# Optimization experiments

Hardware: AMD Instinct MI355X
Metric: run time of the kernel (lower is better)

Reference implementation:

```python
import jax, jax.numpy as jnp
import numpy as np
import math


def setup_inputs() -> dict:
    key = jax.random.key(0)
    ks = jax.random.split(key, 5)
    B, L, H = 16384, 336, 168
    T = L + H
    T_air = jax.random.normal(ks[0], (B, T), dtype=jnp.float32) * 8.0 + 10.0
    T_obs = T_air + jax.random.normal(ks[1], (B, T), dtype=jnp.float32) * 2.0
    wind = jax.random.uniform(ks[2], (B, T), dtype=jnp.float32) * 10.0
    par = jax.random.uniform(ks[3], (B, T), dtype=jnp.float32) * 500.0
    dt = jax.random.uniform(ks[4], (B, T), dtype=jnp.float32) * 3600.0 + 1800.0
    k_init = 1e-4
    k_raw = jnp.float32(k_init + math.log(-math.expm1(-k_init)))  # softplus inverse
    return {
        "T_obs": T_obs, "T_air": T_air, "wind": wind, "par": par, "dt": dt,
        "L_hist": L,
        "k_raw": k_raw,
        "log_q": jnp.float32(-8.0), "log_r": jnp.float32(-4.0),
        "log_p0": jnp.float32(-2.0), "log_q_scale": jnp.float32(0.0),
        "theta_par_lin": jnp.float32(1e-5), "theta_par_quad": jnp.float32(1e-8),
        "theta_wind_cool": jnp.float32(-1e-5), "theta_sensible": jnp.float32(-1e-6),
        "theta_forced_conv": jnp.float32(-1e-7),
    }


def reference(T_obs, T_air, wind, par, dt, L_hist, k_raw, log_q, log_r, log_p0,
              log_q_scale, theta_par_lin, theta_par_quad, theta_wind_cool,
              theta_sensible, theta_forced_conv):
    B, T_total = T_obs.shape
    L = int(L_hist)
    H = T_total - L

    k = jax.nn.softplus(k_raw)
    q = jnp.exp(log_q)
    q_scale = jnp.exp(log_q_scale)
    R = jnp.exp(log_r)
    P0 = jnp.exp(log_p0)

    def predict(T, P, Ta, w, p, dtt):
        dT = T - Ta
        cl = (theta_par_lin * p + theta_par_quad * p * p + theta_wind_cool * w
              + theta_sensible * dT + theta_forced_conv * w * dT)
        T_pred = jnp.clip(T - k * dT * dtt + cl * dtt, -50.0, 100.0)
        F = jnp.clip(1.0 - k * dtt + (theta_sensible + theta_forced_conv * w) * dtt, -2.0, 2.0)
        P_pred = jnp.clip(F * F * P + q_scale * q * dtt, 1e-10, 1e6)
        return T_pred, P_pred

    def filt_step(carry, xs):
        T, P = carry
        Ta, w, p, dtt, y = xs
        Tp, Pp = predict(T, P, Ta, w, p, dtt)
        S = Pp + R
        K = Pp / S
        T_upd = Tp + K * (y - Tp)
        P_upd = (1.0 - K) ** 2 * Pp + K * K * R
        return (T_upd, P_upd), None

    s0 = T_obs[:, 0]
    P0b = jnp.broadcast_to(P0, (B,)).astype(T_obs.dtype)

    # filtering over t = 1 .. L-1 (forcing from t-1, dt/obs at t)
    filt_xs = (T_air[:, :L - 1].T, wind[:, :L - 1].T, par[:, :L - 1].T,
               jnp.clip(dt[:, 1:L], 1.0, None).T, T_obs[:, 1:L].T)
    (s, P), _ = jax.lax.scan(filt_step, (s0, P0b), filt_xs)

    def fcst_step(carry, xs):
        T, P = carry
        Ta, w, p, dtt = xs
        Tp, Pp = predict(T, P, Ta, w, p, dtt)
        return (Tp, Pp), (Tp, Pp)

    # open-loop forecast over t = L .. L+H-1 (forcing from idx-1)
    fcst_xs = (T_air[:, L - 1:L + H - 1].T, wind[:, L - 1:L + H - 1].T,
               par[:, L - 1:L + H - 1].T, jnp.clip(dt[:, L:], 1.0, None).T)
    _, (T_preds, T_vars) = jax.lax.scan(fcst_step, (s, P), fcst_xs)

    return T_preds.T, T_vars.T  # each [B, H]
```

## Files before the change

### kernel.cpp

```cpp
#include <hip/hip_runtime.h>
#include <hip/hip_fp16.h>

namespace {
constexpr int kB = 16384;
constexpr int kL = 336;
constexpr int kH = 168;
constexpr int kT = 504;
constexpr int kW = 16;
constexpr int kNW = 32;
constexpr int kFW = 21;
constexpr int kIS = 66;
constexpr int kITile = kW * kIS;
constexpr int kOS = 17;
constexpr int kOTile = 64 * kOS;
}

__device__ inline void fwait(int* f, int target) {
    int guard = 0;
    while (__hip_atomic_load(f, __ATOMIC_ACQUIRE, __HIP_MEMORY_SCOPE_WORKGROUP) < target) {
        __builtin_amdgcn_s_sleep(1);
        if (++guard > (1 << 22)) break;
    }
}
__device__ inline void fpost(int* f, int lane) {
    __threadfence_block();
    if (lane == 0) atomicAdd(f, 1);
}

__global__ __launch_bounds__(256, 1)
void kf_fused(const float* __restrict__ g_obs,
              const float* __restrict__ g_air,
              const float* __restrict__ g_wind,
              const float* __restrict__ g_par,
              const float* __restrict__ g_dt,
              const float* __restrict__ s_k_raw,
              const float* __restrict__ s_log_q,
              const float* __restrict__ s_log_r,
              const float* __restrict__ s_log_p0,
              const float* __restrict__ s_log_qs,
              const float* __restrict__ s_th_pl,
              const float* __restrict__ s_th_pq,
              const float* __restrict__ s_th_wc,
              const float* __restrict__ s_th_s,
              const float* __restrict__ s_th_fc,
              float* __restrict__ out)
{
    __shared__ __half s_in[5][2][kITile];
    __shared__ float  s_oT[2][kOTile];
    __shared__ float  s_oV[2][kOTile];
    __shared__ int    s_flag[8];

    const int tid = threadIdx.x, wid = tid >> 6, lane = tid & 63;
    const int b0 = blockIdx.x * 64;

    if (tid < 8) s_flag[tid] = 0;
    __syncthreads();

    int* pcAW = &s_flag[0];
    int* pcPD = &s_flag[1];
    int* pcY  = &s_flag[2];
    int* cc   = &s_flag[3];
    int* sc   = &s_flag[4];

    if (wid == 1 || wid == 2) {
        const float* g0 = (wid == 1) ? g_air  : g_par;
        const float* g1 = (wid == 1) ? g_wind : g_dt;
        __half* base0 = (wid == 1) ? &s_in[0][0][0] : &s_in[2][0][0];
        __half* base1 = (wid == 1) ? &s_in[1][0][0] : &s_in[3][0][0];
        int* pc = (wid == 1) ? pcAW : pcPD;
        const int rloc = lane >> 4, trel = lane & 15;
        for (int w = 0; w < kNW; ++w) {
            if (w >= 2) fwait(cc, w - 1);
            const int bi = w & 1;
            int t = w * kW + trel; if (t > kT - 1) t = kT - 1;
            float v0[16], v1[16];
#pragma unroll
            for (int i = 0; i < 16; ++i) {
                const size_t off = (size_t)(b0 + 4 * i + rloc) * kT + t;
                v0[i] = g0[off];
                v1[i] = g1[off];
            }
            __half* d0 = base0 + bi * kITile;
            __half* d1 = base1 + bi * kITile;
#pragma unroll
            for (int i = 0; i < 16; ++i) {
                const int idx = trel * kIS + 4 * i + rloc;
                d0[idx] = __float2half(v0[i]);
                d1[idx] = __float2half(v1[i]);
            }
            fpost(pc, lane);
        }
    } else if (wid == 3) {
        const int rloc = lane >> 4, trel = lane & 15;
        for (int w = 0; w < kFW; ++w) {
            if (w >= 2) fwait(cc, w - 1);
            const int bi = w & 1;
            const int t = w * kW + trel;
            float v[16];
#pragma unroll
            for (int i = 0; i < 16; ++i)
                v[i] = g_obs[(size_t)(b0 + 4 * i + rloc) * kT + t];
            __half* d = &s_in[4][bi][0];
#pragma unroll
            for (int i = 0; i < 16; ++i)
                d[trel * kIS + 4 * i + rloc] = __float2half(v[i]);
            fpost(pcY, lane);
        }
        const int rq = lane & 3, rr = lane >> 2;
        float* outT = out;
        float* outV = out + (size_t)kB * kH;
        for (int w = kFW; w < kNW; ++w) {
            fwait(cc, w + 1);
            const int bi = w & 1;
            const int h0 = (w - kFW) * kW;
            const int nq = (w == kNW - 1) ? 2 : 4;
#pragma unroll
            for (int i = 0; i < 4; ++i) {
                const int r = 16 * i + rr;
                if (rq < nq) {
                    const float4 tv = *(const float4*)&s_oT[bi][r * kOS + rq * 4];
                    const float4 vv = *(const float4*)&s_oV[bi][r * kOS + rq * 4];
                    *(float4*)&outT[(size_t)(b0 + r) * kH + h0 + rq * 4] = tv;
                    *(float4*)&outV[(size_t)(b0 + r) * kH + h0 + rq * 4] = vv;
                }
            }
            fpost(sc, lane);
        }
    } else {
        const float kpar = log1pf(expf(s_k_raw[0]));
        const float qq   = expf(s_log_q[0]) * expf(s_log_qs[0]);
        const float R    = expf(s_log_r[0]);
        float P          = expf(s_log_p0[0]);
        const float th_pl = s_th_pl[0], th_pq = s_th_pq[0], th_wc = s_th_wc[0];
        const float th_s  = s_th_s[0],  th_fc = s_th_fc[0];
        float Tst = 0.0f, aC = 0.0f, wC = 0.0f, pC = 0.0f;

        for (int w = 0; w < kNW; ++w) {
            const int bi = w & 1;
            fwait(pcAW, w + 1);
            fwait(pcPD, w + 1);
            if (w < kFW) fwait(pcY, w + 1);
            if (w >= kFW + 2) fwait(sc, w - (kFW + 1));

            const __half* A  = &s_in[0][bi][0];
            const __half* Wd = &s_in[1][bi][0];
            const __half* Pr = &s_in[2][bi][0];
            const __half* Dd = &s_in[3][bi][0];
            const __half* Yy = &s_in[4][bi][0];

            if (w < kFW) {
                int trel = 0;
                if (w == 0) {
                    Tst = __half2float(Yy[lane]);
                    aC  = __half2float(A[lane]);
                    wC  = __half2float(Wd[lane]);
                    pC  = __half2float(Pr[lane]);
                    trel = 1;
                }
                for (; trel < kW; ++trel) {
                    const int ix = trel * kIS + lane;
                    const float dtt = fmaxf(__half2float(Dd[ix]), 1.0f);
                    const float y   = __half2float(Yy[ix]);
                    const float a   = __half2float(A[ix]);
                    const float wv  = __half2float(Wd[ix]);
                    const float pv  = __half2float(Pr[ix]);
                    const float dT  = Tst - aC;
                    const float gk  = fmaf(th_fc, wC, th_s) - kpar;
                    const float base = fmaf(pC, fmaf(th_pq, pC, th_pl), th_wc * wC);
                    const float Tp = fminf(fmaxf(fmaf(fmaf(gk, dT, base), dtt, Tst), -50.0f), 100.0f);
                    const float F  = fminf(fmaxf(fmaf(gk, dtt, 1.0f), -2.0f), 2.0f);
                    const float Pp = fminf(fmaxf(fmaf(F * F, P, qq * dtt), 1e-10f), 1e6f);
                    const float Kg = Pp * __builtin_amdgcn_rcpf(Pp + R);
                    Tst = fmaf(Kg, y - Tp, Tp);
                    const float omk = 1.0f - Kg;
                    P = fmaf(omk * omk, Pp, Kg * Kg * R);
                    aC = a; wC = wv; pC = pv;
                }
            } else {
                float* oT = &s_oT[bi][lane * kOS];
                float* oV = &s_oV[bi][lane * kOS];
#pragma unroll
                for (int trel = 0; trel < kW; ++trel) {
                    const int ix = trel * kIS + lane;
                    const float dtt = fmaxf(__half2float(Dd[ix]), 1.0f);
                    const float a   = __half2float(A[ix]);
                    const float wv  = __half2float(Wd[ix]);
                    const float pv  = __half2float(Pr[ix]);
                    const float dT  = Tst - aC;
                    const float gk  = fmaf(th_fc, wC, th_s) - kpar;
                    const float base = fmaf(pC, fmaf(th_pq, pC, th_pl), th_wc * wC);
                    Tst = fminf(fmaxf(fmaf(fmaf(gk, dT, base), dtt, Tst), -50.0f), 100.0f);
                    const float F = fminf(fmaxf(fmaf(gk, dtt, 1.0f), -2.0f), 2.0f);
                    P = fminf(fmaxf(fmaf(F * F, P, qq * dtt), 1e-10f), 1e6f);
                    oT[trel] = Tst;
                    oV[trel] = P;
                    aC = a; wC = wv; pC = pv;
                }
            }
            fpost(cc, lane);
        }
    }
}

extern "C" void kernel_launch(void* const* d_in, const int* in_sizes, int n_in,
                              void* d_out, int out_size, void* d_ws, size_t ws_size,
                              hipStream_t stream) {
    const float* g_obs  = (const float*)d_in[0];
    const float* g_air  = (const float*)d_in[1];
    const float* g_wind = (const float*)d_in[2];
    const float* g_par  = (const float*)d_in[3];
    const float* g_dt   = (const float*)d_in[4];
    const float* k_raw  = (const float*)d_in[6];
    const float* log_q  = (const float*)d_in[7];
    const float* log_r  = (const float*)d_in[8];
    const float* log_p0 = (const float*)d_in[9];
    const float* log_qs = (const float*)d_in[10];
    const float* th_pl  = (const float*)d_in[11];
    const float* th_pq  = (const float*)d_in[12];
    const float* th_wc  = (const float*)d_in[13];
    const float* th_s   = (const float*)d_in[14];
    const float* th_fc  = (const float*)d_in[15];
    float* out = (float*)d_out;

    dim3 grid(kB / 64), block(256);
    hipLaunchKernelGGL(kf_fused, grid, block, 0, stream,
                       g_obs, g_air, g_wind, g_par, g_dt,
                       k_raw, log_q, log_r, log_p0, log_qs,
                       th_pl, th_pq, th_wc, th_s, th_fc, out);
}
```

Measured before the change: 220.5 us.

## Prefetch inputs two windows ahead with float4 loads and relax flag fences

Loader wavefronts now issue float4 global loads for the next two time windows into registers before waiting, so global latency overlaps with the compute wave's work. Shared staging moves from fp16 to fp32, which removes the conversions and the precision loss but doubles LDS use. The workgroup fences and acquire loads on the flags are replaced with relaxed atomics plus an explicit lgkmcnt wait and compiler barriers, which cuts synchronisation overhead but relies on those ordering assumptions being correct.

```diff
diff --git a/kernel.cpp b/kernel.cpp
--- a/kernel.cpp
+++ b/kernel.cpp
@@ -1,5 +1,4 @@
 #include <hip/hip_runtime.h>
-#include <hip/hip_fp16.h>
 
 namespace {
 constexpr int kB = 16384;
@@ -17,14 +16,16 @@
 
 __device__ inline void fwait(int* f, int target) {
     int guard = 0;
-    while (__hip_atomic_load(f, __ATOMIC_ACQUIRE, __HIP_MEMORY_SCOPE_WORKGROUP) < target) {
+    while (__hip_atomic_load(f, __ATOMIC_RELAXED, __HIP_MEMORY_SCOPE_WORKGROUP) < target) {
         __builtin_amdgcn_s_sleep(1);
         if (++guard > (1 << 22)) break;
     }
+    asm volatile("" ::: "memory");
 }
 __device__ inline void fpost(int* f, int lane) {
-    __threadfence_block();
-    if (lane == 0) atomicAdd(f, 1);
+    asm volatile("s_waitcnt lgkmcnt(0)" ::: "memory");
+    if (lane == 0)
+        __hip_atomic_fetch_add(f, 1, __ATOMIC_RELAXED, __HIP_MEMORY_SCOPE_WORKGROUP);
 }
 
 __global__ __launch_bounds__(256, 1)
@@ -45,10 +46,10 @@
               const float* __restrict__ s_th_fc,
               float* __restrict__ out)
 {
-    __shared__ __half s_in[5][2][kITile];
-    __shared__ float  s_oT[2][kOTile];
-    __shared__ float  s_oV[2][kOTile];
-    __shared__ int    s_flag[8];
+    __shared__ float s_in[5][2][kITile];
+    __shared__ float s_oT[2][kOTile];
+    __shared__ float s_oV[2][kOTile];
+    __shared__ int   s_flag[8];
 
     const int tid = threadIdx.x, wid = tid >> 6, lane = tid & 63;
     const int b0 = blockIdx.x * 64;
@@ -62,49 +63,68 @@
     int* cc   = &s_flag[3];
     int* sc   = &s_flag[4];
 
+    const int iq = lane & 3;
+    const int ir = lane >> 2;
+
+    auto issue = [&](const float* __restrict__ g, int w, float4* r) {
+        int t = w * kW + iq * 4;
+        if (t > kT - 4) t = kT - 4;
+#pragma unroll
+        for (int i = 0; i < 4; ++i)
+            r[i] = *(const float4*)(g + (size_t)(b0 + 16 * i + ir) * kT + t);
+    };
+    auto stash = [&](const float4* r, float* dst) {
+        const int tb = iq * 4;
+#pragma unroll
+        for (int i = 0; i < 4; ++i) {
+            const int row = 16 * i + ir;
+            dst[(tb + 0) * kIS + row] = r[i].x;
+            dst[(tb + 1) * kIS + row] = r[i].y;
+            dst[(tb + 2) * kIS + row] = r[i].z;
+            dst[(tb + 3) * kIS + row] = r[i].w;
+        }
+    };
+
     if (wid == 1 || wid == 2) {
         const float* g0 = (wid == 1) ? g_air  : g_par;
         const float* g1 = (wid == 1) ? g_wind : g_dt;
-        __half* base0 = (wid == 1) ? &s_in[0][0][0] : &s_in[2][0][0];
-        __half* base1 = (wid == 1) ? &s_in[1][0][0] : &s_in[3][0][0];
+        float* base0 = (wid == 1) ? &s_in[0][0][0] : &s_in[2][0][0];
+        float* base1 = (wid == 1) ? &s_in[1][0][0] : &s_in[3][0][0];
         int* pc = (wid == 1) ? pcAW : pcPD;
-        const int rloc = lane >> 4, trel = lane & 15;
+
+        float4 a0[4], b0r[4], a1[4], b1r[4];
+        issue(g0, 0, a0); issue(g1, 0, b0r);
+        issue(g0, 1, a1); issue(g1, 1, b1r);
+        __builtin_amdgcn_sched_barrier(0);
         for (int w = 0; w < kNW; ++w) {
             if (w >= 2) fwait(cc, w - 1);
-            const int bi = w & 1;
-            int t = w * kW + trel; if (t > kT - 1) t = kT - 1;
-            float v0[16], v1[16];
-#pragma unroll
-            for (int i = 0; i < 16; ++i) {
-                const size_t off = (size_t)(b0 + 4 * i + rloc) * kT + t;
-                v0[i] = g0[off];
-                v1[i] = g1[off];
-            }
-            __half* d0 = base0 + bi * kITile;
-            __half* d1 = base1 + bi * kITile;
-#pragma unroll
-            for (int i = 0; i < 16; ++i) {
-                const int idx = trel * kIS + 4 * i + rloc;
-                d0[idx] = __float2half(v0[i]);
-                d1[idx] = __float2half(v1[i]);
-            }
-            fpost(pc, lane);
+            if (w & 1) {
+                stash(a1, base0 + kITile); stash(b1r, base1 + kITile);
+                fpost(pc, lane);
+                if (w + 2 < kNW) { issue(g0, w + 2, a1); issue(g1, w + 2, b1r); }
+            } else {
+                stash(a0, base0); stash(b0r, base1);
+                fpost(pc, lane);
+                if (w + 2 < kNW) { issue(g0, w + 2, a0); issue(g1, w + 2, b0r); }
+            }
+            __builtin_amdgcn_sched_barrier(0);
         }
     } else if (wid == 3) {
-        const int rloc = lane >> 4, trel = lane & 15;
+        float4 y0[4], y1[4];
+        issue(g_obs, 0, y0); issue(g_obs, 1, y1);
+        __builtin_amdgcn_sched_barrier(0);
         for (int w = 0; w < kFW; ++w) {
             if (w >= 2) fwait(cc, w - 1);
-            const int bi = w & 1;
-            const int t = w * kW + trel;
-            float v[16];
-#pragma unroll
-            for (int i = 0; i < 16; ++i)
-                v[i] = g_obs[(size_t)(b0 + 4 * i + rloc) * kT + t];
-            __half* d = &s_in[4][bi][0];
-#pragma unroll
-            for (int i = 0; i < 16; ++i)
-                d[trel * kIS + 4 * i + rloc] = __float2half(v[i]);
-            fpost(pcY, lane);
+            if (w & 1) {
+                stash(y1, &s_in[4][1][0]);
+                fpost(pcY, lane);
+                if (w + 2 < kFW) issue(g_obs, w + 2, y1);
+            } else {
+                stash(y0, &s_in[4][0][0]);
+                fpost(pcY, lane);
+                if (w + 2 < kFW) issue(g_obs, w + 2, y0);
+            }
+            __builtin_amdgcn_sched_barrier(0);
         }
         const int rq = lane & 3, rr = lane >> 2;
         float* outT = out;
@@ -142,28 +162,23 @@
             if (w < kFW) fwait(pcY, w + 1);
             if (w >= kFW + 2) fwait(sc, w - (kFW + 1));
 
-            const __half* A  = &s_in[0][bi][0];
-            const __half* Wd = &s_in[1][bi][0];
-            const __half* Pr = &s_in[2][bi][0];
-            const __half* Dd = &s_in[3][bi][0];
-            const __half* Yy = &s_in[4][bi][0];
+            const float* A  = &s_in[0][bi][0];
+            const float* Wd = &s_in[1][bi][0];
+            const float* Pr = &s_in[2][bi][0];
+            const float* Dd = &s_in[3][bi][0];
+            const float* Yy = &s_in[4][bi][0];
 
             if (w < kFW) {
                 int trel = 0;
                 if (w == 0) {
-                    Tst = __half2float(Yy[lane]);
-                    aC  = __half2float(A[lane]);
-                    wC  = __half2float(Wd[lane]);
-                    pC  = __half2float(Pr[lane]);
+                    Tst = Yy[lane]; aC = A[lane]; wC = Wd[lane]; pC = Pr[lane];
                     trel = 1;
                 }
                 for (; trel < kW; ++trel) {
                     const int ix = trel * kIS + lane;
-                    const float dtt = fmaxf(__half2float(Dd[ix]), 1.0f);
-                    const float y   = __half2float(Yy[ix]);
-                    const float a   = __half2float(A[ix]);
-                    const float wv  = __half2float(Wd[ix]);
-                    const float pv  = __half2float(Pr[ix]);
+                    const float dtt = fmaxf(Dd[ix], 1.0f);
+                    const float y   = Yy[ix];
+                    const float a = A[ix], wv = Wd[ix], pv = Pr[ix];
                     const float dT  = Tst - aC;
                     const float gk  = fmaf(th_fc, wC, th_s) - kpar;
                     const float base = fmaf(pC, fmaf(th_pq, pC, th_pl), th_wc * wC);
@@ -182,10 +197,8 @@
 #pragma unroll
                 for (int trel = 0; trel < kW; ++trel) {
                     const int ix = trel * kIS + lane;
-                    const float dtt = fmaxf(__half2float(Dd[ix]), 1.0f);
-                    const float a   = __half2float(A[ix]);
-                    const float wv  = __half2float(Wd[ix]);
-                    const float pv  = __half2float(Pr[ix]);
+                    const float dtt = fmaxf(Dd[ix], 1.0f);
+                    const float a = A[ix], wv = Wd[ix], pv = Pr[ix];
                     const float dT  = Tst - aC;
                     const float gk  = fmaf(th_fc, wC, th_s) - kpar;
                     const float base = fmaf(pC, fmaf(th_pq, pC, th_pl), th_wc * wC);
```

New measurement: 219.5 us. No clear change (-0.5%).
